# Performance work log

Measured on AMD Instinct MI355X. Metric: run time of the kernel, lower is better.

Reference implementation:

```python
import jax, jax.numpy as jnp
import numpy as np

D_EMB = 1024
N_HEADS = 16
HEAD_SIZE = 64
LN_EPS = 1e-5


def _layernorm(x, g, b):
    mu = jnp.mean(x, axis=-1, keepdims=True)
    var = jnp.var(x, axis=-1, keepdims=True)
    return (x - mu) * jax.lax.rsqrt(var + LN_EPS) * g + b


def setup_inputs() -> dict:
    key = jax.random.key(0)
    ks = jax.random.split(key, 16)
    B, N, D, H, HS = 8, 1024, D_EMB, N_HEADS, HEAD_SIZE
    s_in = 1.0 / np.sqrt(D)
    s_h = 1.0 / np.sqrt(H * HS)
    s_ff = 1.0 / np.sqrt(4 * D)
    return {
        "x": jax.random.normal(ks[0], (B, N, D), jnp.float32),
        # per-head q/k/v projections, stacked over heads: [H, D, HS]
        "Wq": jax.random.normal(ks[1], (H, D, HS), jnp.float32) * s_in,
        "bq": jnp.zeros((H, HS), jnp.float32),
        "Wk": jax.random.normal(ks[2], (H, D, HS), jnp.float32) * s_in,
        "bk": jnp.zeros((H, HS), jnp.float32),
        "Wv": jax.random.normal(ks[3], (H, D, HS), jnp.float32) * s_in,
        "bv": jnp.zeros((H, HS), jnp.float32),
        "Wproj": jax.random.normal(ks[4], (H * HS, D), jnp.float32) * s_h,
        "bproj": jnp.zeros((D,), jnp.float32),
        "W1": jax.random.normal(ks[5], (D, 4 * D), jnp.float32) * s_in,
        "b1": jnp.zeros((4 * D,), jnp.float32),
        "W2": jax.random.normal(ks[6], (4 * D, D), jnp.float32) * s_ff,
        "b2": jnp.zeros((D,), jnp.float32),
        "ln1_g": jnp.ones((D,), jnp.float32),
        "ln1_b": jnp.zeros((D,), jnp.float32),
        "ln2_g": jnp.ones((D,), jnp.float32),
        "ln2_b": jnp.zeros((D,), jnp.float32),
    }


def reference(x, Wq, bq, Wk, bk, Wv, bv, Wproj, bproj, W1, b1, W2, b2,
              ln1_g, ln1_b, ln2_g, ln2_b):
    # --- pre-LN multi-head attention (dropout = identity in eval) ---
    h = _layernorm(x, ln1_g, ln1_b)                    # [B, N, D]
    q = jnp.einsum('bnd,hds->bhns', h, Wq) + bq[None, :, None, :]
    k = jnp.einsum('bnd,hds->bhns', h, Wk) + bk[None, :, None, :]
    v = jnp.einsum('bnd,hds->bhns', h, Wv) + bv[None, :, None, :]
    scale = 1.0 / jnp.sqrt(jnp.float32(HEAD_SIZE))
    wei = jnp.einsum('bhns,bhms->bhnm', q, k) * scale  # [B, H, N, N]
    wei = jax.nn.softmax(wei, axis=-1)
    attn = jnp.einsum('bhnm,bhms->bhns', wei, v)       # [B, H, N, HS]
    B, H, N, HS = attn.shape
    attn = attn.transpose(0, 2, 1, 3).reshape(B, N, H * HS)  # concat heads
    x = x + attn @ Wproj + bproj
    # --- pre-LN feed-forward with LeakyReLU ---
    h2 = _layernorm(x, ln2_g, ln2_b)
    ff = jax.nn.leaky_relu(h2 @ W1 + b1, negative_slope=0.01) @ W2 + b2
    return x + ff
```

## Files before the change

### kernel.cpp

```cpp
#include <hip/hip_runtime.h>
#include <cstdint>
#include <cstddef>

typedef unsigned short u16;
typedef __attribute__((ext_vector_type(4))) float f32x4;
typedef __attribute__((ext_vector_type(8))) short s16x8;

#define D_EMB 1024
#define NSEQ 1024
#define NB 8
#define NH 16
#define HS 64
#define DFF 4096
#define MTOT (NB*NSEQ)

__device__ __forceinline__ u16 f2bf(float f){
  unsigned u = __float_as_uint(f);
  u += 0x7FFFu + ((u >> 16) & 1u);
  return (u16)(u >> 16);
}

__device__ __forceinline__ void gload_lds16(const void* g, void* l){
  __builtin_amdgcn_global_load_lds((const __attribute__((address_space(1))) void*)g,
                                   (__attribute__((address_space(3))) void*)l, 16, 0, 0);
}

__global__ void transpose_cvt(const float* __restrict__ in, u16* __restrict__ out,
                              int R, int C, size_t inStride, size_t outStride){
  __shared__ float t[32][33];
  const float* ip = in + (size_t)blockIdx.z * inStride;
  u16* op = out + (size_t)blockIdx.z * outStride;
  int c0 = blockIdx.x * 32, r0 = blockIdx.y * 32;
  int tx = threadIdx.x, ty = threadIdx.y;
#pragma unroll
  for (int j = 0; j < 32; j += 8)
    t[ty + j][tx] = ip[(size_t)(r0 + ty + j) * C + (c0 + tx)];
  __syncthreads();
#pragma unroll
  for (int j = 0; j < 32; j += 8)
    op[(size_t)(c0 + ty + j) * R + (r0 + tx)] = f2bf(t[tx][ty + j]);
}

__global__ __launch_bounds__(256) void ln_kernel(const float* __restrict__ x,
    const float* __restrict__ g, const float* __restrict__ bb, u16* __restrict__ out){
  int row = blockIdx.x;
  const float* xr = x + (size_t)row * D_EMB;
  int c = threadIdx.x * 4;
  f32x4 v = *(const f32x4*)(xr + c);
  float s1 = v[0] + v[1] + v[2] + v[3];
  float s2 = v[0]*v[0] + v[1]*v[1] + v[2]*v[2] + v[3]*v[3];
#pragma unroll
  for (int m = 32; m > 0; m >>= 1){ s1 += __shfl_xor(s1, m); s2 += __shfl_xor(s2, m); }
  __shared__ float ps1[4], ps2[4];
  int w = threadIdx.x >> 6;
  if ((threadIdx.x & 63) == 0){ ps1[w] = s1; ps2[w] = s2; }
  __syncthreads();
  s1 = ps1[0] + ps1[1] + ps1[2] + ps1[3];
  s2 = ps2[0] + ps2[1] + ps2[2] + ps2[3];
  float mu = s1 * (1.f / D_EMB);
  float var = s2 * (1.f / D_EMB) - mu * mu;
  float rs = rsqrtf(var + 1e-5f);
  ushort4 o;
  o.x = f2bf((v[0]-mu)*rs*g[c+0] + bb[c+0]);
  o.y = f2bf((v[1]-mu)*rs*g[c+1] + bb[c+1]);
  o.z = f2bf((v[2]-mu)*rs*g[c+2] + bb[c+2]);
  o.w = f2bf((v[3]-mu)*rs*g[c+3] + bb[c+3]);
  *(ushort4*)(out + (size_t)row * D_EMB + c) = o;
}

template<int MODE, int BNT>
__global__ __launch_bounds__(512) void gemm256(
    const u16* __restrict__ A, const u16* __restrict__ Bt,
    int M, int N, int K,
    const float* __restrict__ bias0, const float* __restrict__ bias1,
    const float* __restrict__ bias2, const float* __restrict__ resid,
    void* __restrict__ o0, void* __restrict__ o1, void* __restrict__ o2)
{
  constexpr int BMT = 256;
  constexpr int WCN = BNT/64, WRN = 8/WCN;
  constexpr int WROWS = BMT/WRN;
  constexpr int RF = WROWS/16, RH = RF/2;
  constexpr int ALD = 2, BLD = (BNT*32)/(512*8);
  constexpr int AHALF = BMT*32, BHALF = BNT*32;
  extern __shared__ u16 lds[];
  u16* const Ab = lds;
  u16* const Bb = lds + 4*AHALF;

  const int tid = threadIdx.x;
  const int wid = tid>>6, lane = tid&63, lr = lane&15, lg = lane>>4;
  const int wr = wid/WCN, wc = wid%WCN;

  const int gx = gridDim.x;
  const int nwg = gx * gridDim.y;
  const int bid = blockIdx.x + blockIdx.y*gx;
  const int wg = (bid&7)*(nwg>>3) + (bid>>3);
  const int m0 = (wg % gx) * BMT;
  const int n0 = (wg / gx) * BNT;

  const int nkt = K/64;
  const int srow = tid>>2;
  const int sl = (tid&3) ^ ((tid>>2)&3);

  auto stageA = [&](int nb, int kt1, int kh){
    const u16* src = A + (size_t)m0 * K + (size_t)kt1*64 + kh*32 + sl*8;
    u16* dst = Ab + (nb*2 + kh)*AHALF + tid*8;
#pragma unroll
    for (int r = 0; r < ALD; ++r)
      gload_lds16(src + (size_t)(r*128 + srow)*K, dst + r*4096);
  };
  auto stageB = [&](int nb, int kt1, int kh){
    const u16* src = Bt + (size_t)n0 * K + (size_t)kt1*64 + kh*32 + sl*8;
    u16* dst = Bb + (nb*2 + kh)*BHALF + tid*8;
#pragma unroll
    for (int r = 0; r < BLD; ++r)
      gload_lds16(src + (size_t)(r*128 + srow)*K, dst + r*4096);
  };
  auto rdA = [&](int cur, int kh, int fm) -> s16x8 {
    const int row = wr*WROWS + fm*16 + lr;
    return *(const s16x8*)&Ab[(cur*2+kh)*AHALF + row*32 + ((lg ^ (row&3))<<3)];
  };
  auto rdB = [&](int cur, int kh, int fn) -> s16x8 {
    const int row = wc*64 + fn*16 + lr;
    return *(const s16x8*)&Bb[(cur*2+kh)*BHALF + row*32 + ((lg ^ (row&3))<<3)];
  };
  auto waitv = [&](){
    if constexpr (ALD + BLD == 4) asm volatile("s_waitcnt vmcnt(4)" ::: "memory");
    else                          asm volatile("s_waitcnt vmcnt(3)" ::: "memory");
  };

  f32x4 acc[RF][4];
#pragma unroll
  for (int i = 0; i < RF; i++)
#pragma unroll
    for (int j = 0; j < 4; j++) acc[i][j] = {0.f,0.f,0.f,0.f};

  stageA(0,0,0); stageB(0,0,0); stageA(0,0,1); stageB(0,0,1);
  waitv();
  __builtin_amdgcn_s_barrier();

  s16x8 bf[4];
  for (int kt = 0; kt < nkt; ++kt){
    const int cur = kt&1, nb = cur^1;
    const bool st = (kt+1 < nkt);
#pragma unroll
    for (int kh = 0; kh < 2; ++kh){
      s16x8 af[RH];
#pragma unroll
      for (int j = 0; j < RH; ++j) af[j] = rdA(cur, kh, j);
#pragma unroll
      for (int fn = 0; fn < 4; ++fn) bf[fn] = rdB(cur, kh, fn);
      if (st){ if (kh == 0) stageA(nb, kt+1, 0); else stageA(nb, kt+1, 1); }
      __builtin_amdgcn_s_barrier();
      asm volatile("s_waitcnt lgkmcnt(0)" ::: "memory");
      __builtin_amdgcn_sched_barrier(0);
      __builtin_amdgcn_s_setprio(1);
#pragma unroll
      for (int j = 0; j < RH; ++j)
#pragma unroll
        for (int fn = 0; fn < 4; ++fn)
          acc[j][fn] = __builtin_amdgcn_mfma_f32_16x16x32_bf16(af[j], bf[fn], acc[j][fn], 0, 0, 0);
      __builtin_amdgcn_s_setprio(0);
      __builtin_amdgcn_s_barrier();
#pragma unroll
      for (int j = 0; j < RH; ++j) af[j] = rdA(cur, kh, RH + j);
      if (st){ if (kh == 0) stageB(nb, kt+1, 0); else stageB(nb, kt+1, 1); }
      __builtin_amdgcn_s_barrier();
      asm volatile("s_waitcnt lgkmcnt(0)" ::: "memory");
      __builtin_amdgcn_sched_barrier(0);
      __builtin_amdgcn_s_setprio(1);
#pragma unroll
      for (int j = 0; j < RH; ++j)
#pragma unroll
        for (int fn = 0; fn < 4; ++fn)
          acc[RH+j][fn] = __builtin_amdgcn_mfma_f32_16x16x32_bf16(af[j], bf[fn], acc[RH+j][fn], 0, 0, 0);
      __builtin_amdgcn_s_setprio(0);
      if (kh == 0){
        if (st) waitv();
        else    asm volatile("s_waitcnt vmcnt(0)" ::: "memory");
      } else {
        if (st) waitv();
      }
      __builtin_amdgcn_s_barrier();
    }
  }

#pragma unroll
  for (int fm = 0; fm < RF; fm++){
    const int gmb = m0 + wr*WROWS + fm*16 + lg*4;
#pragma unroll
    for (int fn = 0; fn < 4; fn++){
      const int gn = n0 + wc*64 + fn*16 + lr;
#pragma unroll
      for (int i = 0; i < 4; i++){
        const int gm = gmb + i;
        float v = acc[fm][fn][i];
        if (MODE == 0){
          const int cls = gn >> 10, nn = gn & 1023;
          if (cls == 0)      ((u16*)o0)[(size_t)gm * D_EMB + nn] = f2bf(v + bias0[nn]);
          else if (cls == 1) ((u16*)o1)[(size_t)gm * D_EMB + nn] = f2bf(v + bias1[nn]);
          else {
            const int hh = nn >> 6, ss = nn & 63, bb = gm >> 10, tt = gm & 1023;
            ((u16*)o2)[(((size_t)(bb * NH + hh)) * HS + ss) * NSEQ + tt] = f2bf(v + bias2[nn]);
          }
        } else if (MODE == 1){
          ((float*)o0)[(size_t)gm * N + gn] = resid[(size_t)gm * N + gn] + v + bias0[gn];
        } else {
          float y = v + bias0[gn];
          y = y > 0.f ? y : 0.01f * y;
          ((u16*)o0)[(size_t)gm * N + gn] = f2bf(y);
        }
      }
    }
  }
}

#define BM 128
#define BN 128
#define BK 32
template<int MODE>
__global__ __launch_bounds__(256) void gemm_bt(
    const u16* __restrict__ A, const u16* __restrict__ Bt,
    int M, int N, int K,
    const float* __restrict__ bias0, const float* __restrict__ bias1,
    const float* __restrict__ bias2, const float* __restrict__ resid,
    void* __restrict__ o0, void* __restrict__ o1, void* __restrict__ o2)
{
  __shared__ alignas(16) u16 Al[2][BM*BK];
  __shared__ alignas(16) u16 Bl[2][BN*BK];
  const int tid = threadIdx.x;
  const int m0 = blockIdx.x * BM, n0 = blockIdx.y * BN;
  const int wid = tid >> 6, lane = tid & 63;
  const int wm = (wid >> 1) * 64, wn = (wid & 1) * 64;
  const int lr = lane & 15, lg = lane >> 4;

  f32x4 acc[4][4];
#pragma unroll
  for (int i = 0; i < 4; i++)
#pragma unroll
    for (int j = 0; j < 4; j++) acc[i][j] = {0.f,0.f,0.f,0.f};

  const int nk = K / BK;
  const int arow = tid >> 2, akg = tid & 3;

  auto stage = [&](int bufi, int kt){
    const int k0 = kt * BK;
    const u16* ap = A  + (size_t)(m0 + arow) * K + k0 + akg * 8;
    gload_lds16(ap,                  &Al[bufi][tid * 8]);
    gload_lds16(ap + (size_t)64 * K, &Al[bufi][2048 + tid * 8]);
    const u16* bp = Bt + (size_t)(n0 + arow) * K + k0 + akg * 8;
    gload_lds16(bp,                  &Bl[bufi][tid * 8]);
    gload_lds16(bp + (size_t)64 * K, &Bl[bufi][2048 + tid * 8]);
  };

  stage(0, 0);
  for (int kt = 0; kt < nk; ++kt){
    __syncthreads();
    if (kt + 1 < nk) stage((kt + 1) & 1, kt + 1);
    const int bufi = kt & 1;
    s16x8 af[4], bfr[4];
#pragma unroll
    for (int i = 0; i < 4; i++){
      af[i]  = *(const s16x8*)&Al[bufi][(wm + i*16 + lr) * BK + lg * 8];
      bfr[i] = *(const s16x8*)&Bl[bufi][(wn + i*16 + lr) * BK + lg * 8];
    }
#pragma unroll
    for (int i = 0; i < 4; i++)
#pragma unroll
      for (int j = 0; j < 4; j++)
        acc[i][j] = __builtin_amdgcn_mfma_f32_16x16x32_bf16(af[i], bfr[j], acc[i][j], 0, 0, 0);
  }

#pragma unroll
  for (int fm = 0; fm < 4; fm++){
    const int gmb = m0 + wm + fm * 16 + lg * 4;
#pragma unroll
    for (int fn = 0; fn < 4; fn++){
      const int gn = n0 + wn + fn * 16 + lr;
#pragma unroll
      for (int i = 0; i < 4; i++){
        const int gm = gmb + i;
        float v = acc[fm][fn][i];
        if (MODE == 0){
          const int cls = gn >> 10, nn = gn & 1023;
          if (cls == 0)      ((u16*)o0)[(size_t)gm * D_EMB + nn] = f2bf(v + bias0[nn]);
          else if (cls == 1) ((u16*)o1)[(size_t)gm * D_EMB + nn] = f2bf(v + bias1[nn]);
          else {
            const int hh = nn >> 6, ss = nn & 63, bb = gm >> 10, tt = gm & 1023;
            ((u16*)o2)[(((size_t)(bb * NH + hh)) * HS + ss) * NSEQ + tt] = f2bf(v + bias2[nn]);
          }
        } else if (MODE == 1){
          ((float*)o0)[(size_t)gm * N + gn] = resid[(size_t)gm * N + gn] + v + bias0[gn];
        } else {
          float y = v + bias0[gn];
          y = y > 0.f ? y : 0.01f * y;
          ((u16*)o0)[(size_t)gm * N + gn] = f2bf(y);
        }
      }
    }
  }
}

__global__ __launch_bounds__(256) void attn_kernel(
    const u16* __restrict__ Qb, const u16* __restrict__ Kb, const u16* __restrict__ VT,
    u16* __restrict__ attnC)
{
  const int bid = blockIdx.x;
  const int bh = bid & 127, qt = bid >> 7;
  const int b = bh >> 4, h = bh & 15;
  const int tid = threadIdx.x, w = tid >> 6, lane = tid & 63;
  const int lr = lane & 15, lg = lane >> 4;
  const int q0 = qt * 128 + w * 32;

  __shared__ alignas(16) u16 Kl[2][64*64];
  __shared__ alignas(16) u16 Vl[2][64*64];
  __shared__ alignas(16) u16 Pl[4][32][72];

  const int srow = tid >> 3, scg = tid & 7;
  const u16* kbase = Kb + (size_t)(b * NSEQ) * D_EMB + h * HS;
  const u16* vbase = VT + ((size_t)(b * NH + h)) * HS * NSEQ;

  auto stage = [&](int buf, int kt){
    const int tk = kt * 64;
#pragma unroll
    for (int p = 0; p < 2; ++p){
      const int row = srow + p * 32;
      const int sc = scg ^ (row & 7);
      gload_lds16(kbase + (size_t)(tk + row) * D_EMB + sc * 8, &Kl[buf][(p * 256 + tid) * 8]);
      gload_lds16(vbase + (size_t)row * NSEQ + tk + sc * 8,    &Vl[buf][(p * 256 + tid) * 8]);
    }
  };

  s16x8 aq[2][2];
#pragma unroll
  for (int rb = 0; rb < 2; rb++)
#pragma unroll
    for (int kh = 0; kh < 2; kh++)
      aq[rb][kh] = *(const s16x8*)(Qb + (size_t)(b * NSEQ + q0 + rb * 16 + lr) * D_EMB
                                   + h * HS + kh * 32 + lg * 8);

  float m_i[2][4], l_i[2][4];
  f32x4 zero = {0.f, 0.f, 0.f, 0.f};
  f32x4 ao[2][4];
#pragma unroll
  for (int rb = 0; rb < 2; rb++)
#pragma unroll
    for (int i = 0; i < 4; i++){ m_i[rb][i] = -1e30f; l_i[rb][i] = 0.f; ao[rb][i] = zero; }

  const float scale = 0.125f;
  const int rsw = lr & 7;

  stage(0, 0);
  for (int kt = 0; kt < NSEQ / 64; ++kt){
    __syncthreads();
    if (kt + 1 < NSEQ / 64) stage((kt + 1) & 1, kt + 1);
    const int cur = kt & 1;

    f32x4 sv[2][4];
#pragma unroll
    for (int rb = 0; rb < 2; rb++)
#pragma unroll
      for (int fn = 0; fn < 4; fn++) sv[rb][fn] = zero;
#pragma unroll
    for (int fn = 0; fn < 4; fn++){
      const int krow = fn * 16 + lr;
#pragma unroll
      for (int kh = 0; kh < 2; kh++){
        const int chunk = (kh * 4 + lg) ^ rsw;
        s16x8 kf = *(const s16x8*)&Kl[cur][krow * 64 + chunk * 8];
        sv[0][fn] = __builtin_amdgcn_mfma_f32_16x16x32_bf16(aq[0][kh], kf, sv[0][fn], 0, 0, 0);
        sv[1][fn] = __builtin_amdgcn_mfma_f32_16x16x32_bf16(aq[1][kh], kf, sv[1][fn], 0, 0, 0);
      }
    }

#pragma unroll
    for (int rb = 0; rb < 2; rb++){
      float p[4][4];
#pragma unroll
      for (int i = 0; i < 4; i++){
        float s0 = sv[rb][0][i] * scale, s1 = sv[rb][1][i] * scale;
        float s2 = sv[rb][2][i] * scale, s3 = sv[rb][3][i] * scale;
        float rmax = fmaxf(fmaxf(s0, s1), fmaxf(s2, s3));
#pragma unroll
        for (int mm = 8; mm > 0; mm >>= 1) rmax = fmaxf(rmax, __shfl_xor(rmax, mm));
        float mnew = fmaxf(m_i[rb][i], rmax);
        float fac = __expf(m_i[rb][i] - mnew);
        float p0 = __expf(s0 - mnew), p1 = __expf(s1 - mnew);
        float p2 = __expf(s2 - mnew), p3 = __expf(s3 - mnew);
        p[0][i] = p0; p[1][i] = p1; p[2][i] = p2; p[3][i] = p3;
        float rs = (p0 + p1) + (p2 + p3);
#pragma unroll
        for (int mm = 8; mm > 0; mm >>= 1) rs += __shfl_xor(rs, mm);
        l_i[rb][i] = l_i[rb][i] * fac + rs;
        m_i[rb][i] = mnew;
#pragma unroll
        for (int fn = 0; fn < 4; fn++) ao[rb][fn][i] *= fac;
      }
#pragma unroll
      for (int fn = 0; fn < 4; fn++)
#pragma unroll
        for (int i = 0; i < 4; i++)
          Pl[w][rb * 16 + lg * 4 + i][fn * 16 + lr] = f2bf(p[fn][i]);
    }

    s16x8 vf[4][2];
#pragma unroll
    for (int fn = 0; fn < 4; fn++){
      const int vrow = fn * 16 + lr;
#pragma unroll
      for (int kh = 0; kh < 2; kh++){
        const int chunk = (kh * 4 + lg) ^ rsw;
        vf[fn][kh] = *(const s16x8*)&Vl[cur][vrow * 64 + chunk * 8];
      }
    }
#pragma unroll
    for (int rb = 0; rb < 2; rb++){
      s16x8 pa0 = *(const s16x8*)&Pl[w][rb * 16 + lr][lg * 8];
      s16x8 pa1 = *(const s16x8*)&Pl[w][rb * 16 + lr][32 + lg * 8];
#pragma unroll
      for (int fn = 0; fn < 4; fn++){
        ao[rb][fn] = __builtin_amdgcn_mfma_f32_16x16x32_bf16(pa0, vf[fn][0], ao[rb][fn], 0, 0, 0);
        ao[rb][fn] = __builtin_amdgcn_mfma_f32_16x16x32_bf16(pa1, vf[fn][1], ao[rb][fn], 0, 0, 0);
      }
    }
  }

#pragma unroll
  for (int rb = 0; rb < 2; rb++)
#pragma unroll
    for (int fn = 0; fn < 4; fn++)
#pragma unroll
      for (int i = 0; i < 4; i++){
        float v = ao[rb][fn][i] / l_i[rb][i];
        attnC[(size_t)(b * NSEQ + q0 + rb * 16 + lg * 4 + i) * D_EMB + h * HS + fn * 16 + lr] = f2bf(v);
      }
}

extern "C" void kernel_launch(void* const* d_in, const int* in_sizes, int n_in,
                              void* d_out, int out_size, void* d_ws, size_t ws_size,
                              hipStream_t stream)
{
  const float* x    = (const float*)d_in[0];
  const float* Wq   = (const float*)d_in[1];
  const float* bq   = (const float*)d_in[2];
  const float* Wk   = (const float*)d_in[3];
  const float* bk   = (const float*)d_in[4];
  const float* Wv   = (const float*)d_in[5];
  const float* bv   = (const float*)d_in[6];
  const float* Wp   = (const float*)d_in[7];
  const float* bp   = (const float*)d_in[8];
  const float* W1   = (const float*)d_in[9];
  const float* b1   = (const float*)d_in[10];
  const float* W2   = (const float*)d_in[11];
  const float* b2   = (const float*)d_in[12];
  const float* ln1g = (const float*)d_in[13];
  const float* ln1b = (const float*)d_in[14];
  const float* ln2g = (const float*)d_in[15];
  const float* ln2b = (const float*)d_in[16];
  float* out = (float*)d_out;

  char* ws = (char*)d_ws;
  size_t off = 0;
  auto mk = [&](size_t bytes)->void*{ void* p = ws + off; off += (bytes + 255) & ~(size_t)255; return p; };
  u16*  h1    = (u16*) mk((size_t)MTOT * D_EMB * 2);
  u16*  Qb    = (u16*) mk((size_t)MTOT * D_EMB * 2);
  u16*  Kb    = (u16*) mk((size_t)MTOT * D_EMB * 2);
  u16*  VTb   = (u16*) mk((size_t)MTOT * D_EMB * 2);
  u16*  attnC = (u16*) mk((size_t)MTOT * D_EMB * 2);
  float* x1   = (float*)mk((size_t)MTOT * D_EMB * 4);
  u16*  h2    = (u16*) mk((size_t)MTOT * D_EMB * 2);
  u16*  ffb   = (u16*) mk((size_t)MTOT * DFF * 2);
  u16*  WqkvT = (u16*) mk((size_t)3 * D_EMB * D_EMB * 2);
  u16*  WpT   = (u16*) mk((size_t)D_EMB * D_EMB * 2);
  u16*  W1T   = (u16*) mk((size_t)D_EMB * DFF * 2);
  u16*  W2T   = (u16*) mk((size_t)D_EMB * DFF * 2);

  dim3 tb(32, 8, 1);
  transpose_cvt<<<dim3(HS/32, D_EMB/32, NH), tb, 0, stream>>>(Wq, WqkvT,                         D_EMB, HS, (size_t)D_EMB*HS, (size_t)HS*D_EMB);
  transpose_cvt<<<dim3(HS/32, D_EMB/32, NH), tb, 0, stream>>>(Wk, WqkvT + (size_t)D_EMB*D_EMB,   D_EMB, HS, (size_t)D_EMB*HS, (size_t)HS*D_EMB);
  transpose_cvt<<<dim3(HS/32, D_EMB/32, NH), tb, 0, stream>>>(Wv, WqkvT + (size_t)2*D_EMB*D_EMB, D_EMB, HS, (size_t)D_EMB*HS, (size_t)HS*D_EMB);
  transpose_cvt<<<dim3(D_EMB/32, D_EMB/32, 1), tb, 0, stream>>>(Wp, WpT,  D_EMB, D_EMB, 0, 0);
  transpose_cvt<<<dim3(DFF/32,  D_EMB/32, 1), tb, 0, stream>>>(W1, W1T,  D_EMB, DFF,   0, 0);
  transpose_cvt<<<dim3(D_EMB/32, DFF/32,  1), tb, 0, stream>>>(W2, W2T,  DFF,   D_EMB, 0, 0);

  ln_kernel<<<MTOT, 256, 0, stream>>>(x, ln1g, ln1b, h1);

  bool big = true;
  big &= hipFuncSetAttribute(reinterpret_cast<const void*>(&gemm256<0,256>),
                             hipFuncAttributeMaxDynamicSharedMemorySize, 131072) == hipSuccess;
  big &= hipFuncSetAttribute(reinterpret_cast<const void*>(&gemm256<2,256>),
                             hipFuncAttributeMaxDynamicSharedMemorySize, 131072) == hipSuccess;
  big &= hipFuncSetAttribute(reinterpret_cast<const void*>(&gemm256<1,128>),
                             hipFuncAttributeMaxDynamicSharedMemorySize, 98304) == hipSuccess;

  if (big){
    gemm256<0,256><<<dim3(MTOT/256, 3*D_EMB/256), 512, 131072, stream>>>(h1, WqkvT, MTOT, 3*D_EMB, D_EMB,
        bq, bk, bv, nullptr, Qb, Kb, VTb);
    attn_kernel<<<NB*NH*(NSEQ/128), 256, 0, stream>>>(Qb, Kb, VTb, attnC);
    gemm256<1,128><<<dim3(MTOT/256, D_EMB/128), 512, 98304, stream>>>(attnC, WpT, MTOT, D_EMB, D_EMB,
        bp, nullptr, nullptr, x, x1, nullptr, nullptr);
    ln_kernel<<<MTOT, 256, 0, stream>>>(x1, ln2g, ln2b, h2);
    gemm256<2,256><<<dim3(MTOT/256, DFF/256), 512, 131072, stream>>>(h2, W1T, MTOT, DFF, D_EMB,
        b1, nullptr, nullptr, nullptr, ffb, nullptr, nullptr);
    gemm256<1,128><<<dim3(MTOT/256, D_EMB/128), 512, 98304, stream>>>(ffb, W2T, MTOT, D_EMB, DFF,
        b2, nullptr, nullptr, x1, out, nullptr, nullptr);
  } else {
    gemm_bt<0><<<dim3(MTOT/BM, (3*D_EMB)/BN), 256, 0, stream>>>(h1, WqkvT, MTOT, 3*D_EMB, D_EMB,
        bq, bk, bv, nullptr, Qb, Kb, VTb);
    attn_kernel<<<NB*NH*(NSEQ/128), 256, 0, stream>>>(Qb, Kb, VTb, attnC);
    gemm_bt<1><<<dim3(MTOT/BM, D_EMB/BN), 256, 0, stream>>>(attnC, WpT, MTOT, D_EMB, D_EMB,
        bp, nullptr, nullptr, x, x1, nullptr, nullptr);
    ln_kernel<<<MTOT, 256, 0, stream>>>(x1, ln2g, ln2b, h2);
    gemm_bt<2><<<dim3(MTOT/BM, DFF/BN), 256, 0, stream>>>(h2, W1T, MTOT, DFF, D_EMB,
        b1, nullptr, nullptr, nullptr, ffb, nullptr, nullptr);
    gemm_bt<1><<<dim3(MTOT/BM, D_EMB/BN), 256, 0, stream>>>(ffb, W2T, MTOT, D_EMB, DFF,
        b2, nullptr, nullptr, x1, out, nullptr, nullptr);
  }
}
```

Baseline: 503.8 us.

## Deepen GEMM k-loop prefetch to a 4-slot ring of 32-wide tiles

Replaces the double-buffered 64-wide k-tile loop, where each tile was split into two 32-wide halves, with a 4-slot ring of 32-wide k-tiles. Loads for tile kt+3 are issued while tile kt is computed, and vmcnt waits are adjusted to keep three tiles in flight. The aim is to hide more global-load latency with the same LDS footprint. It also drops the XOR swizzle on LDS reads and writes, which risks more LDS bank conflicts on the fragment reads.

```diff
diff --git a/kernel.cpp b/kernel.cpp
--- a/kernel.cpp
+++ b/kernel.cpp
@@ -24,6 +24,8 @@
   __builtin_amdgcn_global_load_lds((const __attribute__((address_space(1))) void*)g,
                                    (__attribute__((address_space(3))) void*)l, 16, 0, 0);
 }
+
+#define WAITV(n) asm volatile("s_waitcnt vmcnt(" #n ")" ::: "memory")
 
 __global__ void transpose_cvt(const float* __restrict__ in, u16* __restrict__ out,
                               int R, int C, size_t inStride, size_t outStride){
@@ -80,11 +82,13 @@
   constexpr int WCN = BNT/64, WRN = 8/WCN;
   constexpr int WROWS = BMT/WRN;
   constexpr int RF = WROWS/16, RH = RF/2;
-  constexpr int ALD = 2, BLD = (BNT*32)/(512*8);
-  constexpr int AHALF = BMT*32, BHALF = BNT*32;
+  constexpr int ALD = 2;
+  constexpr int BLD = (BNT*32*2)/(512*16);
+  constexpr int PL  = ALD + BLD;
+  constexpr int ABUF = BMT*32, BBUF = BNT*32;
   extern __shared__ u16 lds[];
   u16* const Ab = lds;
-  u16* const Bb = lds + 4*AHALF;
+  u16* const Bb = lds + 4*ABUF;
 
   const int tid = threadIdx.x;
   const int wid = tid>>6, lane = tid&63, lr = lane&15, lg = lane>>4;
@@ -97,35 +101,28 @@
   const int m0 = (wg % gx) * BMT;
   const int n0 = (wg / gx) * BNT;
 
-  const int nkt = K/64;
-  const int srow = tid>>2;
-  const int sl = (tid&3) ^ ((tid>>2)&3);
-
-  auto stageA = [&](int nb, int kt1, int kh){
-    const u16* src = A + (size_t)m0 * K + (size_t)kt1*64 + kh*32 + sl*8;
-    u16* dst = Ab + (nb*2 + kh)*AHALF + tid*8;
-#pragma unroll
-    for (int r = 0; r < ALD; ++r)
-      gload_lds16(src + (size_t)(r*128 + srow)*K, dst + r*4096);
-  };
-  auto stageB = [&](int nb, int kt1, int kh){
-    const u16* src = Bt + (size_t)n0 * K + (size_t)kt1*64 + kh*32 + sl*8;
-    u16* dst = Bb + (nb*2 + kh)*BHALF + tid*8;
-#pragma unroll
-    for (int r = 0; r < BLD; ++r)
-      gload_lds16(src + (size_t)(r*128 + srow)*K, dst + r*4096);
-  };
-  auto rdA = [&](int cur, int kh, int fm) -> s16x8 {
+  const int nkt = K/32;
+  const int srow = tid>>2, sc8 = (tid&3)*8;
+
+  auto stageA = [&](int kt3){
+    const u16* src = A + (size_t)(m0 + srow)*K + kt3*32 + sc8;
+    u16* dst = Ab + (kt3&3)*ABUF + tid*8;
+    gload_lds16(src, dst);
+    gload_lds16(src + (size_t)128*K, dst + 4096);
+  };
+  auto stageB = [&](int kt3){
+    const u16* src = Bt + (size_t)(n0 + srow)*K + kt3*32 + sc8;
+    u16* dst = Bb + (kt3&3)*BBUF + tid*8;
+    gload_lds16(src, dst);
+    if constexpr (BLD == 2) gload_lds16(src + (size_t)128*K, dst + 4096);
+  };
+  auto rdA = [&](int kt, int fm) -> s16x8 {
     const int row = wr*WROWS + fm*16 + lr;
-    return *(const s16x8*)&Ab[(cur*2+kh)*AHALF + row*32 + ((lg ^ (row&3))<<3)];
-  };
-  auto rdB = [&](int cur, int kh, int fn) -> s16x8 {
+    return *(const s16x8*)&Ab[(kt&3)*ABUF + row*32 + lg*8];
+  };
+  auto rdB = [&](int kt, int fn) -> s16x8 {
     const int row = wc*64 + fn*16 + lr;
-    return *(const s16x8*)&Bb[(cur*2+kh)*BHALF + row*32 + ((lg ^ (row&3))<<3)];
-  };
-  auto waitv = [&](){
-    if constexpr (ALD + BLD == 4) asm volatile("s_waitcnt vmcnt(4)" ::: "memory");
-    else                          asm volatile("s_waitcnt vmcnt(3)" ::: "memory");
+    return *(const s16x8*)&Bb[(kt&3)*BBUF + row*32 + lg*8];
   };
 
   f32x4 acc[RF][4];
@@ -134,55 +131,59 @@
 #pragma unroll
     for (int j = 0; j < 4; j++) acc[i][j] = {0.f,0.f,0.f,0.f};
 
-  stageA(0,0,0); stageB(0,0,0); stageA(0,0,1); stageB(0,0,1);
-  waitv();
+  auto tile = [&](int kt, bool doStage, int wsel){
+    s16x8 af[RH], bf[4];
+#pragma unroll
+    for (int j = 0; j < RH; ++j) af[j] = rdA(kt, j);
+#pragma unroll
+    for (int f = 0; f < 4;  ++f) bf[f] = rdB(kt, f);
+    if (doStage) stageA(kt+3);
+    __builtin_amdgcn_s_barrier();
+    asm volatile("s_waitcnt lgkmcnt(0)" ::: "memory");
+    __builtin_amdgcn_sched_barrier(0);
+    __builtin_amdgcn_s_setprio(1);
+#pragma unroll
+    for (int j = 0; j < RH; ++j)
+#pragma unroll
+      for (int f = 0; f < 4; ++f)
+        acc[j][f] = __builtin_amdgcn_mfma_f32_16x16x32_bf16(af[j], bf[f], acc[j][f], 0, 0, 0);
+    __builtin_amdgcn_s_setprio(0);
+    __builtin_amdgcn_s_barrier();
+#pragma unroll
+    for (int j = 0; j < RH; ++j) af[j] = rdA(kt, RH + j);
+    if (doStage) stageB(kt+3);
+    __builtin_amdgcn_s_barrier();
+    asm volatile("s_waitcnt lgkmcnt(0)" ::: "memory");
+    __builtin_amdgcn_sched_barrier(0);
+    __builtin_amdgcn_s_setprio(1);
+#pragma unroll
+    for (int j = 0; j < RH; ++j)
+#pragma unroll
+      for (int f = 0; f < 4; ++f)
+        acc[RH+j][f] = __builtin_amdgcn_mfma_f32_16x16x32_bf16(af[j], bf[f], acc[RH+j][f], 0, 0, 0);
+    __builtin_amdgcn_s_setprio(0);
+    if (wsel == 2){
+      if constexpr (PL == 4) WAITV(8); else WAITV(6);
+      __builtin_amdgcn_s_barrier();
+    } else if (wsel == 1){
+      if constexpr (PL == 4) WAITV(4); else WAITV(3);
+      __builtin_amdgcn_s_barrier();
+    } else if (wsel == 0){
+      WAITV(0);
+      __builtin_amdgcn_s_barrier();
+    }
+  };
+
+  stageA(0 - 3 + 3); stageB(0);
+  stageA(1); stageB(1);
+  stageA(2); stageB(2);
+  if constexpr (PL == 4) WAITV(8); else WAITV(6);
   __builtin_amdgcn_s_barrier();
 
-  s16x8 bf[4];
-  for (int kt = 0; kt < nkt; ++kt){
-    const int cur = kt&1, nb = cur^1;
-    const bool st = (kt+1 < nkt);
-#pragma unroll
-    for (int kh = 0; kh < 2; ++kh){
-      s16x8 af[RH];
-#pragma unroll
-      for (int j = 0; j < RH; ++j) af[j] = rdA(cur, kh, j);
-#pragma unroll
-      for (int fn = 0; fn < 4; ++fn) bf[fn] = rdB(cur, kh, fn);
-      if (st){ if (kh == 0) stageA(nb, kt+1, 0); else stageA(nb, kt+1, 1); }
-      __builtin_amdgcn_s_barrier();
-      asm volatile("s_waitcnt lgkmcnt(0)" ::: "memory");
-      __builtin_amdgcn_sched_barrier(0);
-      __builtin_amdgcn_s_setprio(1);
-#pragma unroll
-      for (int j = 0; j < RH; ++j)
-#pragma unroll
-        for (int fn = 0; fn < 4; ++fn)
-          acc[j][fn] = __builtin_amdgcn_mfma_f32_16x16x32_bf16(af[j], bf[fn], acc[j][fn], 0, 0, 0);
-      __builtin_amdgcn_s_setprio(0);
-      __builtin_amdgcn_s_barrier();
-#pragma unroll
-      for (int j = 0; j < RH; ++j) af[j] = rdA(cur, kh, RH + j);
-      if (st){ if (kh == 0) stageB(nb, kt+1, 0); else stageB(nb, kt+1, 1); }
-      __builtin_amdgcn_s_barrier();
-      asm volatile("s_waitcnt lgkmcnt(0)" ::: "memory");
-      __builtin_amdgcn_sched_barrier(0);
-      __builtin_amdgcn_s_setprio(1);
-#pragma unroll
-      for (int j = 0; j < RH; ++j)
-#pragma unroll
-        for (int fn = 0; fn < 4; ++fn)
-          acc[RH+j][fn] = __builtin_amdgcn_mfma_f32_16x16x32_bf16(af[j], bf[fn], acc[RH+j][fn], 0, 0, 0);
-      __builtin_amdgcn_s_setprio(0);
-      if (kh == 0){
-        if (st) waitv();
-        else    asm volatile("s_waitcnt vmcnt(0)" ::: "memory");
-      } else {
-        if (st) waitv();
-      }
-      __builtin_amdgcn_s_barrier();
-    }
-  }
+  for (int kt = 0; kt < nkt - 3; ++kt) tile(kt, true, 2);
+  tile(nkt-3, false, 1);
+  tile(nkt-2, false, 0);
+  tile(nkt-1, false, -1);
 
 #pragma unroll
   for (int fm = 0; fm < RF; fm++){
```

After: 504.9 us. About the same (+0.2%).
